# Optimization experiments

Measured on AMD Instinct MI355X. Metric: run time of the kernel, lower is better.

Reference implementation:

```python
import jax, jax.numpy as jnp
import numpy as np

N_NODES = 50000
N_EDGES = 800000
C_IN = 32          # in_channels
N_RAD = 8          # num_radial gaussians
RBF_START, RBF_STOP = 0.0, 5.0


def setup_inputs() -> dict:
    key = jax.random.key(0)
    ks = jax.random.split(key, 8)
    x = jax.random.normal(ks[0], (N_NODES, C_IN), dtype=jnp.float32)
    pos = jax.random.normal(ks[1], (N_NODES, 3), dtype=jnp.float32)
    edge_index = jax.random.randint(ks[2], (2, N_EDGES), 0, N_NODES, dtype=jnp.int64)
    # Xavier-uniform-style init for weights
    def xavier(k, shape, fan_in, fan_out):
        lim = np.sqrt(6.0 / (fan_in + fan_out))
        return jax.random.uniform(k, shape, minval=-lim, maxval=lim, dtype=jnp.float32)
    W_tp = xavier(ks[3], (C_IN, N_RAD, C_IN), C_IN, N_RAD * C_IN)
    W1 = xavier(ks[4], (N_RAD * C_IN, C_IN), N_RAD * C_IN, C_IN)
    b1 = jnp.zeros((C_IN,), dtype=jnp.float32)
    W2 = xavier(ks[5], (C_IN, C_IN), C_IN, C_IN)
    b2 = jnp.zeros((C_IN,), dtype=jnp.float32)
    return {"x": x, "pos": pos, "edge_index": edge_index,
            "W_tp": W_tp, "W1": W1, "b1": b1, "W2": W2, "b2": b2}


def _gaussian_smearing(dist):
    # dist: (E,) -> (E, N_RAD)
    centers = jnp.linspace(RBF_START, RBF_STOP, N_RAD)  # (R,)
    width = (RBF_STOP - RBF_START) / (N_RAD - 1)
    scaling = 1.0 / jnp.sqrt(2.0 * jnp.pi)
    d = dist[:, None] - centers[None, :]
    return scaling * jnp.exp(-0.5 * (d / width) ** 2)


def reference(x, pos, edge_index, W_tp, W1, b1, W2, b2):
    row = edge_index[0]  # target (central) nodes
    col = edge_index[1]  # source (neighbor) nodes
    # edge geometry
    edge_vector = pos[row] - pos[col]                       # (E, 3)
    dist = jnp.sqrt(jnp.sum(edge_vector * edge_vector, axis=-1) + 1e-12)  # (E,)
    rbf = _gaussian_smearing(dist)                          # (E, R)
    # tensor product: gather neighbor features, weight by radial basis
    x_j = x[col]                                            # (E, C)
    weighted = jnp.einsum('ec,cro->ero', x_j, W_tp)         # (E, R, C)
    tp = weighted * rbf[:, :, None]                         # (E, R, C)
    # per-edge MLP on flattened tensor-product output
    msg = tp.reshape(tp.shape[0], -1)                       # (E, R*C)
    msg = jax.nn.silu(msg @ W1 + b1)                        # (E, C)
    msg = msg @ W2 + b2                                     # (E, C)
    # scatter-add messages to central nodes, residual update
    agg = jax.ops.segment_sum(msg, row, num_segments=x.shape[0])  # (N, C)
    return x + agg
```

## Files before the change

### kernel.cpp

```cpp
#include <hip/hip_runtime.h>
#include <hip/hip_bf16.h>

#define C 32
#define R 8
#define NPB 32
#define K_ELL 32
#define OVF_CAP 65536

typedef unsigned int u32;
__device__ __forceinline__ float bflo(u32 u) { return __uint_as_float(u << 16); }
__device__ __forceinline__ float bfhi(u32 u) { return __uint_as_float(u & 0xffff0000u); }
__device__ __forceinline__ u32 f2bf_bits(float f) {
    u32 u = __float_as_uint(f);
    u32 lsb = (u >> 16) & 1u;
    return (u + 0x7fffu + lsb) >> 16;
}

__global__ void k_prepM(const float* __restrict__ Wtp, const float* __restrict__ W1,
                        float* __restrict__ M) {
    int idx = blockIdx.x * 256 + threadIdx.x;
    if (idx >= R * C * C) return;
    int r = idx >> 10;
    int c = (idx >> 5) & 31;
    int j = idx & 31;
    float acc = 0.f;
#pragma unroll
    for (int o = 0; o < C; ++o)
        acc = fmaf(Wtp[c * R * C + r * C + o], W1[(r * C + o) * C + j], acc);
    M[idx] = acc;
}

__global__ void k_fused(const float* __restrict__ x, const float* __restrict__ M,
                        __hip_bfloat16* __restrict__ z,
                        const int* __restrict__ ei, const float* __restrict__ pos,
                        int* __restrict__ cnt, int* __restrict__ ovfcnt,
                        uint4* __restrict__ ovf, uint4* __restrict__ rbfs,
                        uint2* __restrict__ ell, int N, int E, int ZB) {
    __shared__ float xs[NPB * C];
    int t = threadIdx.x;
    if ((int)blockIdx.x < ZB) {
        int n0 = blockIdx.x * NPB;
        for (int i = t * 4; i < NPB * C; i += 256 * 4) {
            size_t gbase = (size_t)n0 * C + i;
            float4 v = make_float4(0.f, 0.f, 0.f, 0.f);
            if (gbase + 3 < (size_t)N * C) v = *(const float4*)(x + gbase);
            *(float4*)(xs + i) = v;
        }
        __syncthreads();
        int r = t & 7, j = t >> 3;
        float m[C];
#pragma unroll
        for (int c = 0; c < C; ++c) m[c] = M[r * C * C + c * C + j];
        int nmax = N - n0; if (nmax > NPB) nmax = NPB;
        for (int nn = 0; nn < nmax; ++nn) {
            const float* xp = xs + nn * C;
            float acc = 0.f;
#pragma unroll
            for (int c = 0; c < C; ++c) acc = fmaf(xp[c], m[c], acc);
            z[(size_t)(n0 + nn) * (R * C) + t] = __float2bfloat16(acc);
        }
    } else {
        int i = (blockIdx.x - ZB) * 256 + t;
        if (i < E) {
            int r = ei[i];
            int c = ei[E + i];
            r = ((unsigned)r < (unsigned)N) ? r : 0;
            c = ((unsigned)c < (unsigned)N) ? c : 0;
            float dx = pos[r * 3 + 0] - pos[c * 3 + 0];
            float dy = pos[r * 3 + 1] - pos[c * 3 + 1];
            float dz = pos[r * 3 + 2] - pos[c * 3 + 2];
            float dist = sqrtf(fmaf(dx, dx, fmaf(dy, dy, dz * dz)) + 1e-12f);
            u32 rb[R];
#pragma unroll
            for (int rr = 0; rr < R; ++rr) {
                float tt = (dist - 0.71428573f * (float)rr) * 1.3999999f;
                rb[rr] = f2bf_bits(0.3989423f * __expf(-0.5f * tt * tt));
            }
            uint4 w;
            w.x = rb[0] | (rb[1] << 16);
            w.y = rb[2] | (rb[3] << 16);
            w.z = rb[4] | (rb[5] << 16);
            w.w = rb[6] | (rb[7] << 16);
            rbfs[i] = w;
            int local = atomicAdd(&cnt[r], 1);
            if (local < K_ELL) {
                uint2 v;
                v.x = (u32)c;
                v.y = (u32)i;
                ell[(size_t)r * K_ELL + local] = v;
            } else {
                int q = atomicAdd(ovfcnt, 1);
                if (q < OVF_CAP) ovf[q] = make_uint4((u32)r, (u32)c, (u32)i, 0u);
            }
        }
    }
}

__device__ __forceinline__ float edge_dot(uint4 rb, uint4 zv, float b1j) {
    float h = b1j;
    h = fmaf(bflo(rb.x), bflo(zv.x), h);
    h = fmaf(bfhi(rb.x), bfhi(zv.x), h);
    h = fmaf(bflo(rb.y), bflo(zv.y), h);
    h = fmaf(bfhi(rb.y), bfhi(zv.y), h);
    h = fmaf(bflo(rb.z), bflo(zv.z), h);
    h = fmaf(bfhi(rb.z), bfhi(zv.z), h);
    h = fmaf(bflo(rb.w), bflo(zv.w), h);
    h = fmaf(bfhi(rb.w), bfhi(zv.w), h);
    return h;
}
__device__ __forceinline__ float silu_f(float h) {
    return h * __builtin_amdgcn_rcpf(1.f + __expf(-h));
}

__global__ void k_edge_ell(const int* __restrict__ cnt, const uint2* __restrict__ ell,
                           const uint4* __restrict__ rbfs,
                           const __hip_bfloat16* __restrict__ z,
                           const float* __restrict__ x, const float* __restrict__ b1,
                           const float* __restrict__ W2, const float* __restrict__ b2,
                           float* __restrict__ out, int N) {
    __shared__ float W2s[C * C];
    for (int i = threadIdx.x; i < C * C; i += blockDim.x) W2s[i] = W2[i];
    __syncthreads();
    int gt = blockIdx.x * blockDim.x + threadIdx.x;
    int j = gt & 31;
    int n = gt >> 5;
    if (n >= N) return;
    int deg = cnt[n];
    int m = deg < K_ELL ? deg : K_ELL;
    uint2 pair = make_uint2(0u, 0u);
    if (j < m) pair = ell[(size_t)n * K_ELL + j];
    float b1j = b1[j];
    float acc = 0.f;
    int base = 0;
    for (; base + 4 <= m; base += 4) {
        u32 c0 = __shfl(pair.x, base + 0, 32), e0 = __shfl(pair.y, base + 0, 32);
        u32 c1 = __shfl(pair.x, base + 1, 32), e1 = __shfl(pair.y, base + 1, 32);
        u32 c2 = __shfl(pair.x, base + 2, 32), e2 = __shfl(pair.y, base + 2, 32);
        u32 c3 = __shfl(pair.x, base + 3, 32), e3 = __shfl(pair.y, base + 3, 32);
        uint4 r0 = rbfs[e0];
        uint4 r1 = rbfs[e1];
        uint4 r2 = rbfs[e2];
        uint4 r3 = rbfs[e3];
        uint4 z0 = ((const uint4*)(z + (size_t)c0 * (R * C)))[j];
        uint4 z1 = ((const uint4*)(z + (size_t)c1 * (R * C)))[j];
        uint4 z2 = ((const uint4*)(z + (size_t)c2 * (R * C)))[j];
        uint4 z3 = ((const uint4*)(z + (size_t)c3 * (R * C)))[j];
        float h0 = edge_dot(r0, z0, b1j);
        float h1 = edge_dot(r1, z1, b1j);
        float h2 = edge_dot(r2, z2, b1j);
        float h3 = edge_dot(r3, z3, b1j);
        acc += silu_f(h0) + silu_f(h1) + silu_f(h2) + silu_f(h3);
    }
    for (; base < m; ++base) {
        u32 c0 = __shfl(pair.x, base, 32), e0 = __shfl(pair.y, base, 32);
        uint4 r0 = rbfs[e0];
        uint4 z0 = ((const uint4*)(z + (size_t)c0 * (R * C)))[j];
        acc += silu_f(edge_dot(r0, z0, b1j));
    }
    float v = fmaf((float)deg, b2[j], x[(size_t)n * C + j]);
#pragma unroll
    for (int i = 0; i < C; ++i)
        v = fmaf(__shfl(acc, i, 32), W2s[i * C + j], v);
    out[(size_t)n * C + j] = v;
}

__global__ void k_overflow(const int* __restrict__ ovfcnt, const uint4* __restrict__ ovf,
                           const uint4* __restrict__ rbfs,
                           const __hip_bfloat16* __restrict__ z,
                           const float* __restrict__ b1, const float* __restrict__ W2,
                           float* __restrict__ out, int N) {
    int novf = ovfcnt[0];
    if (novf > OVF_CAP) novf = OVF_CAP;
    int gt = blockIdx.x * blockDim.x + threadIdx.x;
    int j = gt & 31;
    int g = gt >> 5;
    int ngroups = (gridDim.x * blockDim.x) >> 5;
    for (int q = g; q < novf; q += ngroups) {
        uint4 rec = ovf[q];
        u32 row = rec.x, col = rec.y, eid = rec.z;
        uint4 rb = rbfs[eid];
        uint4 zv = ((const uint4*)(z + (size_t)col * (R * C)))[j];
        float sh = silu_f(edge_dot(rb, zv, b1[j]));
        float v = 0.f;
#pragma unroll
        for (int i = 0; i < C; ++i)
            v = fmaf(__shfl(sh, i, 32), W2[i * C + j], v);
        atomicAdd(&out[(size_t)row * C + j], v);
    }
}

__device__ __forceinline__ float rbf_lane(float dist, int r) {
    float t = (dist - 0.71428573f * (float)r) * 1.3999999f;
    return 0.3989423f * __expf(-0.5f * t * t);
}

__global__ void k_edge_direct(const int* __restrict__ ei, const float* __restrict__ pos,
                              const float* __restrict__ x, const float* __restrict__ M,
                              const float* __restrict__ b1,
                              float* __restrict__ agg, float* __restrict__ deg,
                              int E, int N) {
    __shared__ float Ms[R * C * C];
    for (int i = threadIdx.x; i < R * C * C; i += blockDim.x) Ms[i] = M[i];
    __syncthreads();
    int gt = blockIdx.x * blockDim.x + threadIdx.x;
    int j = gt & 31;
    int g = gt >> 5;
    int ngroups = (gridDim.x * blockDim.x) >> 5;
    float b1j = b1[j];
    for (int e = g; e < E; e += ngroups) {
        int row = ei[e];
        int col = ei[E + e];
        row = ((unsigned)row < (unsigned)N) ? row : 0;
        col = ((unsigned)col < (unsigned)N) ? col : 0;
        float dx = pos[row * 3 + 0] - pos[col * 3 + 0];
        float dy = pos[row * 3 + 1] - pos[col * 3 + 1];
        float dz = pos[row * 3 + 2] - pos[col * 3 + 2];
        float dist = sqrtf(fmaf(dx, dx, fmaf(dy, dy, dz * dz)) + 1e-12f);
        float my_rbf = rbf_lane(dist, j & 7);
        float xr[C];
#pragma unroll
        for (int c = 0; c < C; ++c) xr[c] = x[(size_t)col * C + c];
        float h = b1j;
#pragma unroll
        for (int r = 0; r < R; ++r) {
            float s = 0.f;
#pragma unroll
            for (int c = 0; c < C; ++c)
                s = fmaf(xr[c], Ms[r * C * C + c * C + j], s);
            h = fmaf(__shfl(my_rbf, r, 32), s, h);
        }
        float sh = h / (1.f + __expf(-h));
        atomicAdd(&agg[(size_t)row * C + j], sh);
        if (j == 0) atomicAdd(&deg[row], 1.f);
    }
}

__global__ void k_final(const float* __restrict__ x, const float* __restrict__ agg,
                        const float* __restrict__ deg, const float* __restrict__ W2,
                        const float* __restrict__ b2, float* __restrict__ out,
                        int N) {
    int t = threadIdx.x;
    int j = t & 31;
    float w2[C];
#pragma unroll
    for (int i = 0; i < C; ++i) w2[i] = W2[i * C + j];
    float b2j = b2[j];
    int g = (blockIdx.x * blockDim.x + t) >> 5;
    int ngroups = (gridDim.x * blockDim.x) >> 5;
    for (int n = g; n < N; n += ngroups) {
        const float* ap = agg + (size_t)n * C;
        float acc = 0.f;
#pragma unroll
        for (int i = 0; i < C; ++i) acc = fmaf(ap[i], w2[i], acc);
        out[(size_t)n * C + j] = x[(size_t)n * C + j] + acc + deg[n] * b2j;
    }
}

__global__ void k_edge_full(const int* __restrict__ ei, const float* __restrict__ pos,
                            const float* __restrict__ x,
                            const float* __restrict__ Wtp, const float* __restrict__ W1,
                            const float* __restrict__ b1,
                            const float* __restrict__ W2, const float* __restrict__ b2,
                            float* __restrict__ out, int E, int N) {
    __shared__ float Ms[R * C * C];
    __shared__ float W2s[C * C];
    for (int idx = threadIdx.x; idx < R * C * C; idx += blockDim.x) {
        int r = idx >> 10, c = (idx >> 5) & 31, jj = idx & 31;
        float acc = 0.f;
#pragma unroll
        for (int o = 0; o < C; ++o)
            acc = fmaf(Wtp[c * R * C + r * C + o], W1[(r * C + o) * C + jj], acc);
        Ms[idx] = acc;
    }
    for (int idx = threadIdx.x; idx < C * C; idx += blockDim.x) W2s[idx] = W2[idx];
    __syncthreads();
    int gt = blockIdx.x * blockDim.x + threadIdx.x;
    int j = gt & 31;
    int g = gt >> 5;
    int ngroups = (gridDim.x * blockDim.x) >> 5;
    float b1j = b1[j];
    float b2j = b2[j];
    for (int e = g; e < E; e += ngroups) {
        int row = ei[e];
        int col = ei[E + e];
        row = ((unsigned)row < (unsigned)N) ? row : 0;
        col = ((unsigned)col < (unsigned)N) ? col : 0;
        float dx = pos[row * 3 + 0] - pos[col * 3 + 0];
        float dy = pos[row * 3 + 1] - pos[col * 3 + 1];
        float dz = pos[row * 3 + 2] - pos[col * 3 + 2];
        float dist = sqrtf(fmaf(dx, dx, fmaf(dy, dy, dz * dz)) + 1e-12f);
        float my_rbf = rbf_lane(dist, j & 7);
        float xr[C];
#pragma unroll
        for (int c = 0; c < C; ++c) xr[c] = x[(size_t)col * C + c];
        float h = b1j;
#pragma unroll
        for (int r = 0; r < R; ++r) {
            float s = 0.f;
#pragma unroll
            for (int c = 0; c < C; ++c)
                s = fmaf(xr[c], Ms[r * C * C + c * C + j], s);
            h = fmaf(__shfl(my_rbf, r, 32), s, h);
        }
        float sh = h / (1.f + __expf(-h));
        float v = b2j;
#pragma unroll
        for (int i = 0; i < C; ++i)
            v = fmaf(__shfl(sh, i, 32), W2s[i * C + j], v);
        atomicAdd(&out[(size_t)row * C + j], v);
    }
}

__global__ void k_add_x(const float* __restrict__ x, float* __restrict__ out, int total) {
    int i = blockIdx.x * blockDim.x + threadIdx.x;
    int stride = gridDim.x * blockDim.x;
    for (; i < total; i += stride) out[i] += x[i];
}

extern "C" void kernel_launch(void* const* d_in, const int* in_sizes, int n_in,
                              void* d_out, int out_size, void* d_ws, size_t ws_size,
                              hipStream_t stream) {
    const float* x   = (const float*)d_in[0];
    const float* pos = (const float*)d_in[1];
    const int*   ei  = (const int*)d_in[2];
    const float* Wtp = (const float*)d_in[3];
    const float* W1  = (const float*)d_in[4];
    const float* b1  = (const float*)d_in[5];
    const float* W2  = (const float*)d_in[6];
    const float* b2  = (const float*)d_in[7];
    int N = in_sizes[0] / C;
    int E = in_sizes[2] / 2;

    char* ws = (char*)d_ws;
    size_t mBytes   = (size_t)R * C * C * sizeof(float);
    size_t zBytes   = (size_t)N * R * C * sizeof(__hip_bfloat16);
    size_t cntB     = (size_t)N * sizeof(int);
    size_t ovfcB    = 64;
    size_t ovfB     = (size_t)OVF_CAP * 16;
    size_t rbfsB    = (size_t)E * 16;
    size_t ellB     = (size_t)N * K_ELL * 8;
    size_t aggBytes = (size_t)N * (C + 1) * sizeof(float);
    size_t tierANeed = mBytes + zBytes + cntB + ovfcB + ovfB + rbfsB + ellB;
    bool tierA = ws_size >= tierANeed;
    bool tierB = !tierA && ws_size >= mBytes + aggBytes;

    if (tierA) {
        size_t off = 0;
        float*          M      = (float*)(ws + off); off += mBytes;
        __hip_bfloat16* z      = (__hip_bfloat16*)(ws + off); off += zBytes;
        int*            cnt    = (int*)(ws + off); off += cntB;
        int*            ovfcnt = (int*)(ws + off); off += ovfcB;
        uint4*          ovf    = (uint4*)(ws + off); off += ovfB;
        uint4*          rbfs   = (uint4*)(ws + off); off += rbfsB;
        uint2*          ell    = (uint2*)(ws + off);

        hipMemsetAsync(cnt, 0, cntB + ovfcB, stream);
        k_prepM<<<(R * C * C + 255) / 256, 256, 0, stream>>>(Wtp, W1, M);
        int ZB = (N + NPB - 1) / NPB;
        int SB = (E + 255) / 256;
        k_fused<<<ZB + SB, 256, 0, stream>>>(x, M, z, ei, pos, cnt, ovfcnt, ovf,
                                             rbfs, ell, N, E, ZB);
        int blocks = (int)(((size_t)N * 32 + 255) / 256);
        k_edge_ell<<<blocks, 256, 0, stream>>>(cnt, ell, rbfs, z, x, b1, W2, b2,
                                               (float*)d_out, N);
        k_overflow<<<16, 256, 0, stream>>>(ovfcnt, ovf, rbfs, z, b1, W2,
                                           (float*)d_out, N);
    } else if (tierB) {
        float* M   = (float*)ws;
        float* agg = (float*)(ws + mBytes);
        float* deg = agg + (size_t)N * C;
        hipMemsetAsync(agg, 0, aggBytes, stream);
        k_prepM<<<(R * C * C + 255) / 256, 256, 0, stream>>>(Wtp, W1, M);
        k_edge_direct<<<2048, 256, 0, stream>>>(ei, pos, x, M, b1, agg, deg, E, N);
        k_final<<<1024, 256, 0, stream>>>(x, agg, deg, W2, b2, (float*)d_out, N);
    } else {
        hipMemsetAsync(d_out, 0, (size_t)N * C * sizeof(float), stream);
        k_edge_full<<<1024, 256, 0, stream>>>(ei, pos, x, Wtp, W1, b1, W2, b2,
                                              (float*)d_out, E, N);
        k_add_x<<<1024, 256, 0, stream>>>(x, (float*)d_out, N * C);
    }
}
```

Before: 156.2 us.

## Pack bf16 distance into ELL entries and recompute RBF in edge kernel

Removes the per-edge rbfs buffer (16 bytes per edge written then gathered randomly) and shrinks ELL entries from 8 to 4 bytes by packing the 16-bit column index with a bf16-rounded distance. The edge kernel recomputes Gaussian RBF values cooperatively, one lane per (edge, radial) pair, and broadcasts them with shuffles. This trades scattered global traffic for extra exp and shuffle work, lowers distance precision to bf16 before the RBF, and restricts the fast path to N at most 65535.

```diff
diff --git a/kernel.cpp b/kernel.cpp
--- a/kernel.cpp
+++ b/kernel.cpp
@@ -34,8 +34,8 @@
                         __hip_bfloat16* __restrict__ z,
                         const int* __restrict__ ei, const float* __restrict__ pos,
                         int* __restrict__ cnt, int* __restrict__ ovfcnt,
-                        uint4* __restrict__ ovf, uint4* __restrict__ rbfs,
-                        uint2* __restrict__ ell, int N, int E, int ZB) {
+                        uint4* __restrict__ ovf,
+                        u32* __restrict__ ell, int N, int E, int ZB) {
     __shared__ float xs[NPB * C];
     int t = threadIdx.x;
     if ((int)blockIdx.x < ZB) {
@@ -70,50 +70,31 @@
             float dy = pos[r * 3 + 1] - pos[c * 3 + 1];
             float dz = pos[r * 3 + 2] - pos[c * 3 + 2];
             float dist = sqrtf(fmaf(dx, dx, fmaf(dy, dy, dz * dz)) + 1e-12f);
-            u32 rb[R];
-#pragma unroll
-            for (int rr = 0; rr < R; ++rr) {
-                float tt = (dist - 0.71428573f * (float)rr) * 1.3999999f;
-                rb[rr] = f2bf_bits(0.3989423f * __expf(-0.5f * tt * tt));
-            }
-            uint4 w;
-            w.x = rb[0] | (rb[1] << 16);
-            w.y = rb[2] | (rb[3] << 16);
-            w.z = rb[4] | (rb[5] << 16);
-            w.w = rb[6] | (rb[7] << 16);
-            rbfs[i] = w;
             int local = atomicAdd(&cnt[r], 1);
             if (local < K_ELL) {
-                uint2 v;
-                v.x = (u32)c;
-                v.y = (u32)i;
-                ell[(size_t)r * K_ELL + local] = v;
+                ell[(size_t)r * K_ELL + local] = (u32)c | (f2bf_bits(dist) << 16);
             } else {
                 int q = atomicAdd(ovfcnt, 1);
-                if (q < OVF_CAP) ovf[q] = make_uint4((u32)r, (u32)c, (u32)i, 0u);
+                if (q < OVF_CAP)
+                    ovf[q] = make_uint4((u32)r, (u32)c, __float_as_uint(dist), 0u);
             }
         }
     }
 }
 
-__device__ __forceinline__ float edge_dot(uint4 rb, uint4 zv, float b1j) {
-    float h = b1j;
-    h = fmaf(bflo(rb.x), bflo(zv.x), h);
-    h = fmaf(bfhi(rb.x), bfhi(zv.x), h);
-    h = fmaf(bflo(rb.y), bflo(zv.y), h);
-    h = fmaf(bfhi(rb.y), bfhi(zv.y), h);
-    h = fmaf(bflo(rb.z), bflo(zv.z), h);
-    h = fmaf(bfhi(rb.z), bfhi(zv.z), h);
-    h = fmaf(bflo(rb.w), bflo(zv.w), h);
-    h = fmaf(bfhi(rb.w), bfhi(zv.w), h);
-    return h;
+__device__ __forceinline__ float zsl(uint4 zv, int r) {
+    u32 w = (r < 2) ? zv.x : (r < 4) ? zv.y : (r < 6) ? zv.z : zv.w;
+    return (r & 1) ? bfhi(w) : bflo(w);
 }
 __device__ __forceinline__ float silu_f(float h) {
     return h * __builtin_amdgcn_rcpf(1.f + __expf(-h));
 }
-
-__global__ void k_edge_ell(const int* __restrict__ cnt, const uint2* __restrict__ ell,
-                           const uint4* __restrict__ rbfs,
+__device__ __forceinline__ float rbf_at(float dist, int r) {
+    float t = (dist - 0.71428573f * (float)r) * 1.3999999f;
+    return 0.3989423f * __expf(-0.5f * t * t);
+}
+
+__global__ void k_edge_ell(const int* __restrict__ cnt, const u32* __restrict__ ell,
                            const __hip_bfloat16* __restrict__ z,
                            const float* __restrict__ x, const float* __restrict__ b1,
                            const float* __restrict__ W2, const float* __restrict__ b2,
@@ -127,35 +108,43 @@
     if (n >= N) return;
     int deg = cnt[n];
     int m = deg < K_ELL ? deg : K_ELL;
-    uint2 pair = make_uint2(0u, 0u);
-    if (j < m) pair = ell[(size_t)n * K_ELL + j];
+    u32 packv = 0u;
+    if (j < m) packv = ell[(size_t)n * K_ELL + j];
     float b1j = b1[j];
     float acc = 0.f;
     int base = 0;
     for (; base + 4 <= m; base += 4) {
-        u32 c0 = __shfl(pair.x, base + 0, 32), e0 = __shfl(pair.y, base + 0, 32);
-        u32 c1 = __shfl(pair.x, base + 1, 32), e1 = __shfl(pair.y, base + 1, 32);
-        u32 c2 = __shfl(pair.x, base + 2, 32), e2 = __shfl(pair.y, base + 2, 32);
-        u32 c3 = __shfl(pair.x, base + 3, 32), e3 = __shfl(pair.y, base + 3, 32);
-        uint4 r0 = rbfs[e0];
-        uint4 r1 = rbfs[e1];
-        uint4 r2 = rbfs[e2];
-        uint4 r3 = rbfs[e3];
-        uint4 z0 = ((const uint4*)(z + (size_t)c0 * (R * C)))[j];
-        uint4 z1 = ((const uint4*)(z + (size_t)c1 * (R * C)))[j];
-        uint4 z2 = ((const uint4*)(z + (size_t)c2 * (R * C)))[j];
-        uint4 z3 = ((const uint4*)(z + (size_t)c3 * (R * C)))[j];
-        float h0 = edge_dot(r0, z0, b1j);
-        float h1 = edge_dot(r1, z1, b1j);
-        float h2 = edge_dot(r2, z2, b1j);
-        float h3 = edge_dot(r3, z3, b1j);
+        u32 wmy = __shfl(packv, base + (j >> 3), 32);
+        float dmy = __uint_as_float(wmy & 0xffff0000u);
+        float my = rbf_at(dmy, j & 7);
+        u32 w0 = __shfl(packv, base + 0, 32);
+        u32 w1 = __shfl(packv, base + 1, 32);
+        u32 w2 = __shfl(packv, base + 2, 32);
+        u32 w3 = __shfl(packv, base + 3, 32);
+        uint4 z0 = ((const uint4*)(z + (size_t)(w0 & 0xffffu) * (R * C)))[j];
+        uint4 z1 = ((const uint4*)(z + (size_t)(w1 & 0xffffu) * (R * C)))[j];
+        uint4 z2 = ((const uint4*)(z + (size_t)(w2 & 0xffffu) * (R * C)))[j];
+        uint4 z3 = ((const uint4*)(z + (size_t)(w3 & 0xffffu) * (R * C)))[j];
+        float h0 = b1j, h1 = b1j, h2 = b1j, h3 = b1j;
+#pragma unroll
+        for (int r = 0; r < R; ++r) {
+            h0 = fmaf(__shfl(my, 0 * 8 + r, 32), zsl(z0, r), h0);
+            h1 = fmaf(__shfl(my, 1 * 8 + r, 32), zsl(z1, r), h1);
+            h2 = fmaf(__shfl(my, 2 * 8 + r, 32), zsl(z2, r), h2);
+            h3 = fmaf(__shfl(my, 3 * 8 + r, 32), zsl(z3, r), h3);
+        }
         acc += silu_f(h0) + silu_f(h1) + silu_f(h2) + silu_f(h3);
     }
     for (; base < m; ++base) {
-        u32 c0 = __shfl(pair.x, base, 32), e0 = __shfl(pair.y, base, 32);
-        uint4 r0 = rbfs[e0];
-        uint4 z0 = ((const uint4*)(z + (size_t)c0 * (R * C)))[j];
-        acc += silu_f(edge_dot(r0, z0, b1j));
+        u32 w0 = __shfl(packv, base, 32);
+        float d0 = __uint_as_float(w0 & 0xffff0000u);
+        float my = rbf_at(d0, j & 7);
+        uint4 z0 = ((const uint4*)(z + (size_t)(w0 & 0xffffu) * (R * C)))[j];
+        float h0 = b1j;
+#pragma unroll
+        for (int r = 0; r < R; ++r)
+            h0 = fmaf(__shfl(my, r, 32), zsl(z0, r), h0);
+        acc += silu_f(h0);
     }
     float v = fmaf((float)deg, b2[j], x[(size_t)n * C + j]);
 #pragma unroll
@@ -165,7 +154,6 @@
 }
 
 __global__ void k_overflow(const int* __restrict__ ovfcnt, const uint4* __restrict__ ovf,
-                           const uint4* __restrict__ rbfs,
                            const __hip_bfloat16* __restrict__ z,
                            const float* __restrict__ b1, const float* __restrict__ W2,
                            float* __restrict__ out, int N) {
@@ -177,10 +165,15 @@
     int ngroups = (gridDim.x * blockDim.x) >> 5;
     for (int q = g; q < novf; q += ngroups) {
         uint4 rec = ovf[q];
-        u32 row = rec.x, col = rec.y, eid = rec.z;
-        uint4 rb = rbfs[eid];
+        u32 row = rec.x, col = rec.y;
+        float dist = __uint_as_float(rec.z);
+        float my = rbf_at(dist, j & 7);
         uint4 zv = ((const uint4*)(z + (size_t)col * (R * C)))[j];
-        float sh = silu_f(edge_dot(rb, zv, b1[j]));
+        float h = b1[j];
+#pragma unroll
+        for (int r = 0; r < R; ++r)
+            h = fmaf(__shfl(my, r, 32), zsl(zv, r), h);
+        float sh = silu_f(h);
         float v = 0.f;
 #pragma unroll
         for (int i = 0; i < C; ++i)
@@ -337,11 +330,10 @@
     size_t cntB     = (size_t)N * sizeof(int);
     size_t ovfcB    = 64;
     size_t ovfB     = (size_t)OVF_CAP * 16;
-    size_t rbfsB    = (size_t)E * 16;
-    size_t ellB     = (size_t)N * K_ELL * 8;
+    size_t ellB     = (size_t)N * K_ELL * sizeof(u32);
     size_t aggBytes = (size_t)N * (C + 1) * sizeof(float);
-    size_t tierANeed = mBytes + zBytes + cntB + ovfcB + ovfB + rbfsB + ellB;
-    bool tierA = ws_size >= tierANeed;
+    size_t tierANeed = mBytes + zBytes + cntB + ovfcB + ovfB + ellB;
+    bool tierA = (ws_size >= tierANeed) && (N <= 65535);
     bool tierB = !tierA && ws_size >= mBytes + aggBytes;
 
     if (tierA) {
@@ -351,19 +343,18 @@
         int*            cnt    = (int*)(ws + off); off += cntB;
         int*            ovfcnt = (int*)(ws + off); off += ovfcB;
         uint4*          ovf    = (uint4*)(ws + off); off += ovfB;
-        uint4*          rbfs   = (uint4*)(ws + off); off += rbfsB;
-        uint2*          ell    = (uint2*)(ws + off);
+        u32*            ell    = (u32*)(ws + off);
 
         hipMemsetAsync(cnt, 0, cntB + ovfcB, stream);
         k_prepM<<<(R * C * C + 255) / 256, 256, 0, stream>>>(Wtp, W1, M);
         int ZB = (N + NPB - 1) / NPB;
         int SB = (E + 255) / 256;
         k_fused<<<ZB + SB, 256, 0, stream>>>(x, M, z, ei, pos, cnt, ovfcnt, ovf,
-                                             rbfs, ell, N, E, ZB);
+                                             ell, N, E, ZB);
         int blocks = (int)(((size_t)N * 32 + 255) / 256);
-        k_edge_ell<<<blocks, 256, 0, stream>>>(cnt, ell, rbfs, z, x, b1, W2, b2,
+        k_edge_ell<<<blocks, 256, 0, stream>>>(cnt, ell, z, x, b1, W2, b2,
                                                (float*)d_out, N);
-        k_overflow<<<16, 256, 0, stream>>>(ovfcnt, ovf, rbfs, z, b1, W2,
+        k_overflow<<<16, 256, 0, stream>>>(ovfcnt, ovf, z, b1, W2,
                                            (float*)d_out, N);
     } else if (tierB) {
         float* M   = (float*)ws;
```

After: 142.0 us. 9.0% less time.
